# Optimization experiments

Hardware: AMD Instinct MI355X
Metric: run time of the kernel (lower is better)

Reference implementation:

```python
import jax, jax.numpy as jnp
import numpy as np

B, L, D = 2, 2048, 2048        # batch, seqlen, d_model
DIN, N, R, K = 4096, 16, 128, 4  # d_inner, d_state, dt_rank, d_conv


def setup_inputs() -> dict:
    key = jax.random.key(0)
    ks = jax.random.split(key, 9)
    hidden_states = jax.random.normal(ks[0], (B, L, D), dtype=jnp.float32) * 0.02
    in_proj_w = jax.random.normal(ks[1], (2 * DIN, D), dtype=jnp.float32) * (1.0 / np.sqrt(D))
    conv1d_w = jax.random.normal(ks[2], (DIN, K), dtype=jnp.float32) * (1.0 / np.sqrt(DIN))
    x_proj_w = jax.random.normal(ks[3], (R + 2 * N, DIN), dtype=jnp.float32) * (1.0 / np.sqrt(DIN))
    dt_proj_w = jax.random.normal(ks[4], (DIN, R), dtype=jnp.float32) * (1.0 / np.sqrt(R))
    # dt_proj_bias init: inverse-softplus of dt ~ LogUniform(1e-3, 1e-1), as in init_dtprojbias
    dt = jnp.exp(jax.random.uniform(ks[5], (DIN,)) * (np.log(0.1) - np.log(0.001)) + np.log(0.001))
    dt = jnp.clip(dt, 1e-4, None)
    dt_proj_bias = dt + jnp.log(-jnp.expm1(-dt))
    # A_log init: log(arange(1..N)) broadcast over d_inner (init_A)
    A_log = jnp.broadcast_to(jnp.log(jnp.arange(1, N + 1, dtype=jnp.float32)), (DIN, N))
    D_param = jnp.ones((DIN,), dtype=jnp.float32)
    out_proj_w = jax.random.normal(ks[6], (D, DIN), dtype=jnp.float32) * (1.0 / np.sqrt(DIN))
    return {
        "hidden_states": hidden_states, "in_proj_w": in_proj_w, "conv1d_w": conv1d_w,
        "x_proj_w": x_proj_w, "dt_proj_w": dt_proj_w, "dt_proj_bias": dt_proj_bias,
        "A_log": A_log, "D_param": D_param, "out_proj_w": out_proj_w,
    }


def _mamba_forward(hidden_states, in_proj_w, conv1d_w, x_proj_w, dt_proj_w,
                   dt_proj_bias, A_log, D_param, out_proj_w):
    b, l, _ = hidden_states.shape
    # in_proj: (b,l,d_model) -> (b,l,2*d_inner), split into x and gate z
    xz = jnp.einsum("bld,ed->ble", hidden_states, in_proj_w)
    x, z = jnp.split(xz, 2, axis=-1)  # each (b,l,d_inner)

    # depthwise causal conv1d along l, no bias, then SiLU
    xp = jnp.pad(x, ((0, 0), (K - 1, 0), (0, 0)))
    xc = sum(conv1d_w[:, k] * xp[:, k:k + l, :] for k in range(K))  # (b,l,d_inner)
    xc = jax.nn.silu(xc)

    # x_proj -> dt_rank + 2*d_state, split into dt, B, C
    x_dbl = jnp.einsum("bld,ed->ble", xc, x_proj_w)
    dt_r = x_dbl[..., :R]                    # (b,l,R)
    Bc = x_dbl[..., R:R + N]                 # (b,l,N)
    Cc = x_dbl[..., R + N:]                  # (b,l,N)
    delta = jax.nn.softplus(jnp.einsum("blr,dr->bld", dt_r, dt_proj_w) + dt_proj_bias)  # (b,l,d_inner)

    A = -jnp.exp(A_log)  # (d_inner, N)

    # selective scan: h_t = exp(delta_t*A)*h_{t-1} + delta_t*x_t*B_t; y_t = <h_t, C_t>
    def step(h, inp):
        delta_t, B_t, C_t, x_t = inp  # (b,d), (b,n), (b,n), (b,d)
        dA = jnp.exp(delta_t[..., None] * A)                 # (b,d,n)
        h = h * dA + (delta_t * x_t)[..., None] * B_t[:, None, :]
        y_t = jnp.einsum("bdn,bn->bd", h, C_t)
        return h, y_t

    inputs = (jnp.swapaxes(delta, 0, 1), jnp.swapaxes(Bc, 0, 1),
              jnp.swapaxes(Cc, 0, 1), jnp.swapaxes(xc, 0, 1))
    h0 = jnp.zeros((b, DIN, N), dtype=xc.dtype)
    _, y = jax.lax.scan(step, h0, inputs)     # y: (l,b,d_inner)
    y = jnp.swapaxes(y, 0, 1)                 # (b,l,d_inner)

    y = y + xc * D_param                      # skip term
    y = y * jax.nn.silu(z)                    # gating
    return jnp.einsum("bld,ed->ble", y, out_proj_w)  # (b,l,d_model)


def reference(hidden_states, in_proj_w, conv1d_w, x_proj_w, dt_proj_w,
              dt_proj_bias, A_log, D_param, out_proj_w):
    return _mamba_forward(hidden_states, in_proj_w, conv1d_w, x_proj_w, dt_proj_w,
                          dt_proj_bias, A_log, D_param, out_proj_w)
```

## Files before the change

kernel.cpp:

```cpp
#include <hip/hip_runtime.h>
#include <math.h>

#define DIN   4096
#define NST   16
#define RR    128
#define LSEQ  2048
#define NTOK  4096
#define BB    2
#define CHUNK 64
#define NCH   (LSEQ / CHUNK)
#define KSPL  8
#define KC    (DIN / KSPL)

typedef __attribute__((ext_vector_type(8))) short short8;
typedef __attribute__((ext_vector_type(4))) float f32x4;

__device__ __forceinline__ float sigmoidf_(float x) { return 1.f / (1.f + __expf(-x)); }
__device__ __forceinline__ float softplusf_(float x) {
    return fmaxf(x, 0.f) + log1pf(__expf(-fabsf(x)));
}
__device__ __forceinline__ unsigned short f2bf_(float f) {
    unsigned u = __float_as_uint(f);
    return (unsigned short)((u + 0x7FFFu + ((u >> 16) & 1u)) >> 16);
}
__device__ __forceinline__ void gld_lds16_(const unsigned short* g, unsigned short* l) {
    __builtin_amdgcn_global_load_lds((const __attribute__((address_space(1))) unsigned int*)g,
                                     (__attribute__((address_space(3))) unsigned int*)l,
                                     16, 0, 0);
}

__global__ __launch_bounds__(256)
void f2bf_kernel(const float* __restrict__ src, unsigned short* __restrict__ dst, int n8)
{
    int i = blockIdx.x * 256 + threadIdx.x;
    if (i >= n8) return;
    const float4* s = (const float4*)src + 2 * (size_t)i;
    float4 a = s[0], b = s[1];
    union { unsigned short u[8]; uint4 v; } o;
    o.u[0] = f2bf_(a.x); o.u[1] = f2bf_(a.y); o.u[2] = f2bf_(a.z); o.u[3] = f2bf_(a.w);
    o.u[4] = f2bf_(b.x); o.u[5] = f2bf_(b.y); o.u[6] = f2bf_(b.z); o.u[7] = f2bf_(b.w);
    ((uint4*)dst)[i] = o.v;
}

template<int MODE>
__global__ __launch_bounds__(256)
void gemm_mfma_bt(const unsigned short* __restrict__ A, const unsigned short* __restrict__ W,
                  float* __restrict__ C, int K, int ldc,
                  const float* __restrict__ bias, float* __restrict__ C2)
{
    __shared__ unsigned short As[128 * 32];
    __shared__ unsigned short Ws[128 * 32];
    const int tid = threadIdx.x;
    const int bm = blockIdx.y << 7;
    int bn = blockIdx.x << 7;

    const int c0 = tid, c1 = tid + 256;
    const unsigned short* ga0 = A + (size_t)(bm + (c0 >> 2)) * K + (c0 & 3) * 8;
    const unsigned short* ga1 = A + (size_t)(bm + (c1 >> 2)) * K + (c1 & 3) * 8;
    const unsigned short* gw0 = W + (size_t)(bn + (c0 >> 2)) * K + (c0 & 3) * 8;
    const unsigned short* gw1 = W + (size_t)(bn + (c1 >> 2)) * K + (c1 & 3) * 8;
    unsigned short* la0 = &As[c0 * 8];
    unsigned short* la1 = &As[c1 * 8];
    unsigned short* lw0 = &Ws[c0 * 8];
    unsigned short* lw1 = &Ws[c1 * 8];

    const int ln  = tid & 63;
    const int wv  = tid >> 6;
    const int wm  = (wv >> 1) << 6;
    const int wn  = (wv & 1) << 6;
    const int m15 = ln & 15;
    const int q   = ln >> 4;

    f32x4 acc[4][4] = {};

    for (int k0 = 0; k0 < K; k0 += 32) {
        __syncthreads();
        gld_lds16_(ga0, la0); gld_lds16_(ga1, la1);
        gld_lds16_(gw0, lw0); gld_lds16_(gw1, lw1);
        ga0 += 32; ga1 += 32; gw0 += 32; gw1 += 32;
        __syncthreads();
        short8 af[4], wf[4];
        #pragma unroll
        for (int i = 0; i < 4; ++i)
            af[i] = *(const short8*)&As[(wm + i * 16 + m15) * 32 + q * 8];
        #pragma unroll
        for (int j = 0; j < 4; ++j)
            wf[j] = *(const short8*)&Ws[(wn + j * 16 + m15) * 32 + q * 8];
        #pragma unroll
        for (int i = 0; i < 4; ++i)
            #pragma unroll
            for (int j = 0; j < 4; ++j)
                acc[i][j] = __builtin_amdgcn_mfma_f32_16x16x32_bf16(af[i], wf[j],
                                                                    acc[i][j], 0, 0, 0);
    }

    float* Cp = C;
    if (MODE == 2 && bn >= DIN) { Cp = C2; bn -= DIN; }

    #pragma unroll
    for (int i = 0; i < 4; ++i)
        #pragma unroll
        for (int j = 0; j < 4; ++j) {
            int col = bn + wn + j * 16 + m15;
            #pragma unroll
            for (int r = 0; r < 4; ++r) {
                int row = bm + wm + i * 16 + q * 4 + r;
                float v = acc[i][j][r];
                if (MODE == 1) v = softplusf_(v + bias[col]);
                Cp[(size_t)row * ldc + col] = v;
            }
        }
}

__global__ __launch_bounds__(256)
void gemm_kspl_kernel(const float* __restrict__ A, const float* __restrict__ W,
                      float* __restrict__ partial)
{
    __shared__ float As[16][66];
    __shared__ float Ws[16][162];
    const int tid = threadIdx.x;
    const int tx = tid & 15;
    const int ty = tid >> 4;
    const int bm = blockIdx.x << 6;
    const int k0 = blockIdx.y * KC;

    float acc[4][10] = {};

    for (int kt = 0; kt < KC; kt += 16) {
        float2 a2[2];
        #pragma unroll
        for (int i = 0; i < 2; ++i) {
            int idx = tid + 256 * i;
            int row = idx >> 3, kofs = (idx & 7) * 2;
            a2[i] = *(const float2*)&A[(size_t)(bm + row) * DIN + k0 + kt + kofs];
        }
        float2 w2[5];
        #pragma unroll
        for (int i = 0; i < 5; ++i) {
            int idx = tid + 256 * i;
            int wrow = idx >> 3, wk = (idx & 7) * 2;
            w2[i] = *(const float2*)&W[(size_t)wrow * DIN + k0 + kt + wk];
        }
        __syncthreads();
        #pragma unroll
        for (int i = 0; i < 2; ++i) {
            int idx = tid + 256 * i;
            int row = idx >> 3, kofs = (idx & 7) * 2;
            As[kofs][row] = a2[i].x; As[kofs + 1][row] = a2[i].y;
        }
        #pragma unroll
        for (int i = 0; i < 5; ++i) {
            int idx = tid + 256 * i;
            int wrow = idx >> 3, wk = (idx & 7) * 2;
            Ws[wk][wrow] = w2[i].x; Ws[wk + 1][wrow] = w2[i].y;
        }
        __syncthreads();
        #pragma unroll
        for (int kk = 0; kk < 16; ++kk) {
            float2 av0 = *(const float2*)&As[kk][ty * 4];
            float2 av1 = *(const float2*)&As[kk][ty * 4 + 2];
            float a[4] = {av0.x, av0.y, av1.x, av1.y};
            float w[10];
            #pragma unroll
            for (int j = 0; j < 5; ++j) {
                float2 wv = *(const float2*)&Ws[kk][tx * 10 + 2 * j];
                w[2 * j] = wv.x; w[2 * j + 1] = wv.y;
            }
            #pragma unroll
            for (int i = 0; i < 4; ++i)
                #pragma unroll
                for (int j = 0; j < 10; ++j)
                    acc[i][j] = fmaf(a[i], w[j], acc[i][j]);
        }
        __syncthreads();
    }

    float* po = partial + (size_t)blockIdx.y * NTOK * 160;
    #pragma unroll
    for (int i = 0; i < 4; ++i) {
        int r = bm + ty * 4 + i;
        #pragma unroll
        for (int j = 0; j < 5; ++j)
            *(float2*)&po[(size_t)r * 160 + tx * 10 + 2 * j] =
                make_float2(acc[i][2 * j], acc[i][2 * j + 1]);
    }
}

__global__ __launch_bounds__(256)
void kspl_reduce_kernel(const float* __restrict__ partial, float* __restrict__ xdbl,
                        unsigned short* __restrict__ dtr)
{
    int idx = blockIdx.x * 256 + threadIdx.x;
    float s = 0.f;
    #pragma unroll
    for (int k = 0; k < KSPL; ++k)
        s += partial[(size_t)k * NTOK * 160 + idx];
    xdbl[idx] = s;
    int row = idx / 160;
    int col = idx - row * 160;
    if (col < RR) dtr[(size_t)row * RR + col] = f2bf_(s);
}

__global__ __launch_bounds__(256)
void conv_silu_kernel(const float* __restrict__ x, const float* __restrict__ cw,
                      float* __restrict__ xc)
{
    int idx = blockIdx.x * 256 + threadIdx.x;
    int d = idx & (DIN - 1);
    int tok = idx >> 12;
    int t = tok & (LSEQ - 1);
    float w0 = cw[d * 4 + 0], w1 = cw[d * 4 + 1];
    float w2 = cw[d * 4 + 2], w3 = cw[d * 4 + 3];
    const float* xp = x + (size_t)tok * DIN + d;
    float acc = w3 * xp[0];
    if (t >= 1) acc = fmaf(w2, xp[-DIN], acc);
    if (t >= 2) acc = fmaf(w1, xp[-2 * DIN], acc);
    if (t >= 3) acc = fmaf(w0, xp[-3 * DIN], acc);
    xc[idx] = acc * sigmoidf_(acc);
}

__global__ __launch_bounds__(256)
void scan_part1_kernel(const float* __restrict__ delta, const float* __restrict__ xc,
                       const float* __restrict__ xdbl, const float* __restrict__ A_log,
                       float* __restrict__ hloc, float* __restrict__ ssum)
{
    int d = blockIdx.x * 256 + threadIdx.x;
    int c = blockIdx.y;
    int b = blockIdx.z;
    float A[NST], h[NST];
    #pragma unroll
    for (int n = 0; n < NST; ++n) {
        A[n] = -__expf(A_log[d * NST + n]);
        h[n] = 0.f;
    }
    float s = 0.f;
    int tok = b * LSEQ + c * CHUNK;
    for (int t = 0; t < CHUNK; ++t, ++tok) {
        float dv = delta[(size_t)tok * DIN + d];
        float xv = xc[(size_t)tok * DIN + d];
        const float* bc = xdbl + (size_t)tok * 160 + RR;
        float dx = dv * xv;
        s += dv;
        #pragma unroll
        for (int n = 0; n < NST; ++n)
            h[n] = fmaf(h[n], __expf(dv * A[n]), dx * bc[n]);
    }
    size_t base = (size_t)(b * NCH + c) * NST * DIN + d;
    #pragma unroll
    for (int n = 0; n < NST; ++n) hloc[base + (size_t)n * DIN] = h[n];
    ssum[(size_t)(b * NCH + c) * DIN + d] = s;
}

__global__ __launch_bounds__(256)
void scan_part2_kernel(float* __restrict__ hloc, const float* __restrict__ ssum,
                       const float* __restrict__ A_log)
{
    int idx = blockIdx.x * 256 + threadIdx.x;
    int b = idx >> 12;
    int d = idx & (DIN - 1);
    float A[NST], hin[NST];
    #pragma unroll
    for (int n = 0; n < NST; ++n) {
        A[n] = -__expf(A_log[d * NST + n]);
        hin[n] = 0.f;
    }
    for (int c = 0; c < NCH; ++c) {
        size_t base = (size_t)(b * NCH + c) * NST * DIN + d;
        float s = ssum[(size_t)(b * NCH + c) * DIN + d];
        #pragma unroll
        for (int n = 0; n < NST; ++n) {
            float hl = hloc[base + (size_t)n * DIN];
            hloc[base + (size_t)n * DIN] = hin[n];
            hin[n] = fmaf(hin[n], __expf(A[n] * s), hl);
        }
    }
}

__global__ __launch_bounds__(256)
void scan_part3_kernel(const float* __restrict__ delta, float* __restrict__ xcy,
                       const float* __restrict__ xdbl, const float* __restrict__ z,
                       const float* __restrict__ A_log, const float* __restrict__ Dp,
                       const float* __restrict__ hin_buf)
{
    int d = blockIdx.x * 256 + threadIdx.x;
    int c = blockIdx.y;
    int b = blockIdx.z;
    float A[NST], h[NST];
    size_t base = (size_t)(b * NCH + c) * NST * DIN + d;
    #pragma unroll
    for (int n = 0; n < NST; ++n) {
        A[n] = -__expf(A_log[d * NST + n]);
        h[n] = hin_buf[base + (size_t)n * DIN];
    }
    float Dv = Dp[d];
    int tok = b * LSEQ + c * CHUNK;
    for (int t = 0; t < CHUNK; ++t, ++tok) {
        float dv = delta[(size_t)tok * DIN + d];
        float xv = xcy[(size_t)tok * DIN + d];
        float zv = z[(size_t)tok * DIN + d];
        const float* bc = xdbl + (size_t)tok * 160 + RR;
        float dx = dv * xv;
        float y = 0.f;
        #pragma unroll
        for (int n = 0; n < NST; ++n) {
            h[n] = fmaf(h[n], __expf(dv * A[n]), dx * bc[n]);
            y = fmaf(h[n], bc[NST + n], y);
        }
        y = (y + xv * Dv) * (zv * sigmoidf_(zv));
        xcy[(size_t)tok * DIN + d] = y;
    }
}

extern "C" void kernel_launch(void* const* d_in, const int* in_sizes, int n_in,
                              void* d_out, int out_size, void* d_ws, size_t ws_size,
                              hipStream_t stream)
{
    const float* hidden     = (const float*)d_in[0];
    const float* in_proj_w  = (const float*)d_in[1];
    const float* conv_w     = (const float*)d_in[2];
    const float* x_proj_w   = (const float*)d_in[3];
    const float* dt_proj_w  = (const float*)d_in[4];
    const float* dt_bias    = (const float*)d_in[5];
    const float* A_log      = (const float*)d_in[6];
    const float* D_param    = (const float*)d_in[7];
    const float* out_proj_w = (const float*)d_in[8];
    float* out = (float*)d_out;

    const size_t BIG = (size_t)NTOK * DIN * sizeof(float);
    char* ws = (char*)d_ws;
    float* xbuf = (float*)(ws);
    float* xc   = (float*)(ws + BIG);
    float* zbuf = (float*)(ws + 2 * BIG);
    float* xdbl = (float*)(ws + 3 * BIG);
    float* delta = xbuf;

    unsigned short* w_in_bf  = (unsigned short*)xc;
    unsigned short* hid_bf   = (unsigned short*)out;
    unsigned short* y_bf     = (unsigned short*)xbuf;
    unsigned short* w_out_bf = (unsigned short*)zbuf;

    float* xpart = out;
    unsigned short* dtr_bf = (unsigned short*)(out + (size_t)KSPL * NTOK * 160);
    unsigned short* dtw_bf = dtr_bf + (size_t)NTOK * RR;
    float* hloc  = out;
    float* ssum  = out + (size_t)BB * NCH * NST * DIN;

    f2bf_kernel<<<8192, 256, 0, stream>>>(in_proj_w, w_in_bf, (2 * DIN * 2048) / 8);
    f2bf_kernel<<<4096, 256, 0, stream>>>(hidden, hid_bf, (NTOK * 2048) / 8);
    gemm_mfma_bt<2><<<dim3(64, 32), 256, 0, stream>>>(hid_bf, w_in_bf, xbuf,
                                                      2048, DIN, nullptr, zbuf);
    conv_silu_kernel<<<(NTOK * DIN) / 256, 256, 0, stream>>>(xbuf, conv_w, xc);
    gemm_kspl_kernel<<<dim3(NTOK / 64, KSPL), 256, 0, stream>>>(xc, x_proj_w, xpart);
    kspl_reduce_kernel<<<(NTOK * 160) / 256, 256, 0, stream>>>(xpart, xdbl, dtr_bf);
    f2bf_kernel<<<256, 256, 0, stream>>>(dt_proj_w, dtw_bf, (DIN * RR) / 8);
    gemm_mfma_bt<1><<<dim3(32, 32), 256, 0, stream>>>(dtr_bf, dtw_bf, delta,
                                                      RR, DIN, dt_bias, nullptr);
    scan_part1_kernel<<<dim3(DIN / 256, NCH, BB), 256, 0, stream>>>(delta, xc, xdbl,
                                                                    A_log, hloc, ssum);
    scan_part2_kernel<<<(BB * DIN) / 256, 256, 0, stream>>>(hloc, ssum, A_log);
    scan_part3_kernel<<<dim3(DIN / 256, NCH, BB), 256, 0, stream>>>(delta, xc, xdbl,
                                                                    zbuf, A_log, D_param, hloc);
    f2bf_kernel<<<8192, 256, 0, stream>>>(xc, y_bf, (NTOK * DIN) / 8);
    f2bf_kernel<<<4096, 256, 0, stream>>>(out_proj_w, w_out_bf, (2048 * DIN) / 8);
    gemm_mfma_bt<0><<<dim3(16, 32), 256, 0, stream>>>(y_bf, w_out_bf, out,
                                                      4096, 2048, nullptr, nullptr);
}
```

Measured before the change: 803.6 us.

## Replace in/out projection GEMMs with 256x256-tile pipelined MFMA kernel

```diff
diff --git a/kernel.cpp b/kernel.cpp
--- a/kernel.cpp
+++ b/kernel.cpp
@@ -40,6 +40,144 @@
     o.u[0] = f2bf_(a.x); o.u[1] = f2bf_(a.y); o.u[2] = f2bf_(a.z); o.u[3] = f2bf_(a.w);
     o.u[4] = f2bf_(b.x); o.u[5] = f2bf_(b.y); o.u[6] = f2bf_(b.z); o.u[7] = f2bf_(b.w);
     ((uint4*)dst)[i] = o.v;
+}
+
+
+#define BAR()        asm volatile("s_barrier" ::: "memory")
+#define WAIT_LGKM0() asm volatile("s_waitcnt lgkmcnt(0)" ::: "memory")
+#define WAIT_VM(n)   asm volatile("s_waitcnt vmcnt(" #n ")" ::: "memory")
+
+
+#define RD_A(P, mh) do { _Pragma("unroll") \
+  for (int ii = 0; ii < 4; ++ii) { _Pragma("unroll") \
+    for (int ks = 0; ks < 2; ++ks) \
+      aF[ii][ks] = *(const short8*)((P) + (mh)*8192 + ii*2048 + ks*64); } } while (0)
+
+#define RD_B(P, nh, DST) do { _Pragma("unroll") \
+  for (int jj = 0; jj < 2; ++jj) { _Pragma("unroll") \
+    for (int ks = 0; ks < 2; ++ks) \
+      DST[jj][ks] = *(const short8*)((P) + (nh)*4096 + jj*2048 + ks*64); } } while (0)
+
+#define MFMA_Q(mh, nh, BF) do { __builtin_amdgcn_s_setprio(1); _Pragma("unroll") \
+  for (int ii = 0; ii < 4; ++ii) { _Pragma("unroll") \
+    for (int jj = 0; jj < 2; ++jj) { _Pragma("unroll") \
+      for (int ks = 0; ks < 2; ++ks) \
+        acc[(mh)*4+ii][(nh)*2+jj] = __builtin_amdgcn_mfma_f32_16x16x32_bf16( \
+            aF[ii][ks], BF[jj][ks], acc[(mh)*4+ii][(nh)*2+jj], 0, 0, 0); } } \
+  __builtin_amdgcn_s_setprio(0); } while (0)
+
+#define STGLD(gbase, sbase, h, l, tile) \
+  gld_lds16_(gbase + (size_t)((h)*128 + (l)*64) * K + (size_t)(tile)*64, \
+             (unsigned short*)(sbase + (h)*16384 + (l)*8192))
+
+#define ITER(t, PREF) do { \
+   \
+  RD_A(pA0, 0); RD_B(pB0c, 0, bA); \
+  STGLD(gA0, sA1, 1, 0, (t)+1); STGLD(gA0, sA1, 1, 1, (t)+1); \
+  BAR(); WAIT_LGKM0(); MFMA_Q(0, 0, bA); BAR(); \
+   \
+  RD_B(pB0c, 1, bB); \
+  BAR(); WAIT_LGKM0(); MFMA_Q(0, 1, bB); BAR(); \
+   \
+  RD_A(pA0, 1); \
+  if (PREF) { STGLD(gB0, sB0, 0, 0, (t)+2); STGLD(gB0, sB0, 0, 1, (t)+2); } \
+  BAR(); WAIT_LGKM0(); MFMA_Q(1, 1, bB); BAR(); \
+   \
+  if (PREF) { STGLD(gA0, sA0, 0, 0, (t)+2); STGLD(gA0, sA0, 0, 1, (t)+2); \
+              STGLD(gB0, sB0, 1, 0, (t)+2); STGLD(gB0, sB0, 1, 1, (t)+2); } \
+  BAR(); WAIT_LGKM0(); MFMA_Q(1, 0, bA); \
+  if (PREF) { WAIT_VM(6); } else { WAIT_VM(0); } \
+  BAR(); \
+   \
+  RD_A(pA1, 0); RD_B(pB1c, 0, bA); \
+  if (PREF) { STGLD(gA0, sA0, 1, 0, (t)+2); STGLD(gA0, sA0, 1, 1, (t)+2); } \
+  BAR(); WAIT_LGKM0(); MFMA_Q(0, 0, bA); BAR(); \
+   \
+  RD_B(pB1c, 1, bB); \
+  BAR(); WAIT_LGKM0(); MFMA_Q(0, 1, bB); BAR(); \
+   \
+  RD_A(pA1, 1); \
+  if (PREF) { STGLD(gB0, sB1, 0, 0, (t)+3); STGLD(gB0, sB1, 0, 1, (t)+3); } \
+  BAR(); WAIT_LGKM0(); MFMA_Q(1, 1, bB); BAR(); \
+   \
+  if (PREF) { STGLD(gA0, sA1, 0, 0, (t)+3); STGLD(gA0, sA1, 0, 1, (t)+3); \
+              STGLD(gB0, sB1, 1, 0, (t)+3); STGLD(gB0, sB1, 1, 1, (t)+3); } \
+  BAR(); WAIT_LGKM0(); MFMA_Q(1, 0, bA); \
+  if (PREF) { WAIT_VM(6); } else { WAIT_VM(0); } \
+  BAR(); \
+} while (0)
+
+template<int MODE>
+__global__ __launch_bounds__(512)
+void gemm256(const unsigned short* __restrict__ A, const unsigned short* __restrict__ W,
+             float* __restrict__ C, int K, int ldc, float* __restrict__ C2, int nbx)
+{
+    __shared__ __align__(16) unsigned short sm[65536];
+    char* smb = (char*)sm;
+
+    const int tid = threadIdx.x;
+    const int ln  = tid & 63;
+    const int wv  = tid >> 6;
+    const int wm  = wv >> 2;
+    const int wn  = wv & 3;
+    const int m15 = ln & 15;
+    const int q   = ln >> 4;
+
+    const int nwg = gridDim.x;
+    const int bid = blockIdx.x;
+    const int swz = (bid & 7) * (nwg >> 3) + (bid >> 3);
+    const int bm  = (swz / nbx) << 8;
+    const int bn  = (swz % nbx) << 8;
+
+    const int swzb    = (m15 & 4) << 3;
+    const int ra_base = wm * 16384 + m15 * 128 + ((q * 16) ^ swzb);
+    const int rb_base = wn * 8192  + m15 * 128 + ((q * 16) ^ swzb);
+    const char* pA0  = smb + ra_base;
+    const char* pA1  = smb + 65536 + ra_base;
+    const char* pB0c = smb + 32768 + rb_base;
+    const char* pB1c = smb + 98304 + rb_base;
+
+    char* sA0 = smb +          tid * 16;
+    char* sB0 = smb + 32768  + tid * 16;
+    char* sA1 = smb + 65536  + tid * 16;
+    char* sB1 = smb + 98304  + tid * 16;
+    const int srow  = tid >> 3;
+    const int secol = ((tid & 7) * 8) ^ (((tid >> 5) & 1) * 16);
+    const unsigned short* gA0 = A + (size_t)(bm + srow) * K + secol;
+    const unsigned short* gB0 = W + (size_t)(bn + srow) * K + secol;
+
+    f32x4  acc[8][4] = {};
+    short8 aF[4][2], bA[2][2], bB[2][2];
+
+    const int KT = K >> 6;
+
+    STGLD(gA0, sA0, 0, 0, 0); STGLD(gA0, sA0, 0, 1, 0);
+    STGLD(gA0, sA0, 1, 0, 0); STGLD(gA0, sA0, 1, 1, 0);
+    STGLD(gB0, sB0, 0, 0, 0); STGLD(gB0, sB0, 0, 1, 0);
+    STGLD(gB0, sB0, 1, 0, 0); STGLD(gB0, sB0, 1, 1, 0);
+    STGLD(gA0, sA1, 0, 0, 1); STGLD(gA0, sA1, 0, 1, 1);
+    STGLD(gB0, sB1, 0, 0, 1); STGLD(gB0, sB1, 0, 1, 1);
+    STGLD(gB0, sB1, 1, 0, 1); STGLD(gB0, sB1, 1, 1, 1);
+    WAIT_VM(6);
+    BAR();
+
+    for (int t = 0; t < KT - 2; t += 2) ITER(t, 1);
+    ITER(KT - 2, 0);
+
+    float* Cp = C;
+    int bcol = bn;
+    if (MODE == 2 && bcol >= DIN) { Cp = C2; bcol -= DIN; }
+    #pragma unroll
+    for (int i = 0; i < 8; ++i) {
+        int row = bm + wm * 128 + i * 16 + q * 4;
+        #pragma unroll
+        for (int j = 0; j < 4; ++j) {
+            int col = bcol + wn * 64 + j * 16 + m15;
+            #pragma unroll
+            for (int r = 0; r < 4; ++r)
+                Cp[(size_t)(row + r) * ldc + col] = acc[i][j][r];
+        }
+    }
 }
 
 template<int MODE>
@@ -347,8 +485,7 @@
 
     f2bf_kernel<<<8192, 256, 0, stream>>>(in_proj_w, w_in_bf, (2 * DIN * 2048) / 8);
     f2bf_kernel<<<4096, 256, 0, stream>>>(hidden, hid_bf, (NTOK * 2048) / 8);
-    gemm_mfma_bt<2><<<dim3(64, 32), 256, 0, stream>>>(hid_bf, w_in_bf, xbuf,
-                                                      2048, DIN, nullptr, zbuf);
+    gemm256<2><<<512, 512, 0, stream>>>(hid_bf, w_in_bf, xbuf, 2048, DIN, zbuf, 32);
     conv_silu_kernel<<<(NTOK * DIN) / 256, 256, 0, stream>>>(xbuf, conv_w, xc);
     gemm_kspl_kernel<<<dim3(NTOK / 64, KSPL), 256, 0, stream>>>(xc, x_proj_w, xpart);
     kspl_reduce_kernel<<<(NTOK * 160) / 256, 256, 0, stream>>>(xpart, xdbl, dtr_bf);
@@ -362,6 +499,5 @@
                                                                     zbuf, A_log, D_param, hloc);
     f2bf_kernel<<<8192, 256, 0, stream>>>(xc, y_bf, (NTOK * DIN) / 8);
     f2bf_kernel<<<4096, 256, 0, stream>>>(out_proj_w, w_out_bf, (2048 * DIN) / 8);
-    gemm_mfma_bt<0><<<dim3(16, 32), 256, 0, stream>>>(y_bf, w_out_bf, out,
-                                                      4096, 2048, nullptr, nullptr);
-}
+    gemm256<0><<<128, 512, 0, stream>>>(y_bf, w_out_bf, out, 4096, 2048, nullptr, 8);
+}
```

Result: faster. 781.1 us (-2.8%).
